# Performance work log

Hardware: AMD Instinct MI355X
Metric: run time of the kernel (lower is better)

The kernel has to match this reference:

```python
import jax, jax.numpy as jnp
import numpy as np

EPS_ATTN = 1e-5   # attention denominator eps (module eps)
EPS_LN = 1e-5     # nn.LayerNorm default eps


def _prime(x, proj):
    # Performer FAVOR+ hyperbolic positive features.
    # x: (B,H,L,dh), proj: (dh,m) -> (B,H,L,2m)
    dn = x.shape[-1] ** -0.25
    xn = dn * x
    d = jnp.einsum('bhld,dm->bhlm', xn, proj)
    diag = 0.5 * jnp.sum(xn * xn, axis=-1, keepdims=True)
    return jnp.concatenate([jnp.exp(d - diag), jnp.exp(-d - diag)], axis=-1)


def setup_inputs() -> dict:
    L, B, H, DH, DM, M = 2048, 4, 8, 64, 512, 256
    key = jax.random.key(0)
    k0, k1, k2 = jax.random.split(key, 3)
    h = jax.random.normal(k0, (L, B, DM), jnp.float32)
    w_qkv = jax.random.normal(k1, (H * 3 * DH, DM), jnp.float32) / np.sqrt(DM)
    w_o = jax.random.normal(k2, (DM, H * DH), jnp.float32) / np.sqrt(H * DH)
    ln_gamma = jnp.ones((DM,), jnp.float32)
    ln_beta = jnp.zeros((DM,), jnp.float32)
    # Gaussian orthogonal random matrix (blockwise QR), rows scaled by sqrt(dh)
    rng = np.random.default_rng(0)
    blocks = []
    for _ in range(M // DH):
        g = rng.standard_normal((DH, DH)).astype(np.float32)
        q, _ = np.linalg.qr(g)
        blocks.append(q.T)
    pm = np.concatenate(blocks, axis=0) * np.sqrt(DH)  # (M, DH)
    proj_matrix = jnp.asarray(pm.T.astype(np.float32))  # (DH, M)
    return {"h": h, "w_qkv": w_qkv, "w_o": w_o,
            "ln_gamma": ln_gamma, "ln_beta": ln_beta,
            "proj_matrix": proj_matrix}


def _forward(h, w_qkv, w_o, ln_gamma, ln_beta, proj_matrix):
    L, B, DM = h.shape
    DH, M = proj_matrix.shape
    H = w_qkv.shape[0] // (3 * DH)
    scale = DH ** -0.5

    qkv = (h @ w_qkv.T).reshape(L, B, H, 3 * DH)
    q, k, v = jnp.split(qkv, 3, axis=-1)
    q = jnp.transpose(q, (1, 2, 0, 3))  # (B,H,L,dh)
    k = jnp.transpose(k, (1, 2, 0, 3))
    v = jnp.transpose(v, (1, 2, 0, 3))

    qp = _prime(q, proj_matrix)  # (B,H,L,2M)
    kp = _prime(k, proj_matrix)
    kp = kp / jnp.sum(kp, axis=-1, keepdims=True)
    qp = qp / jnp.sum(qp, axis=-1, keepdims=True)

    den_acc = jnp.cumsum(kp, axis=2)
    denom = jnp.einsum('bhlm,bhlm->bhl', den_acc, qp)[..., None]  # (B,H,L,1)

    # fast_weight_sum: W_t = W_{t-1} + k_t v_t^T ; out_t = q_t @ W_t
    def step(W, xs):
        qt, kt, vt = xs  # (B,H,2M), (B,H,2M), (B,H,dh)
        W = W + kt[..., :, None] * vt[..., None, :]
        out = jnp.einsum('bhm,bhmd->bhd', qt, W)
        return W, out

    W0 = jnp.zeros((B, H, 2 * M, DH), h.dtype)
    xs = (jnp.transpose(qp, (2, 0, 1, 3)),
          jnp.transpose(kp, (2, 0, 1, 3)),
          jnp.transpose(v, (2, 0, 1, 3)))
    _, out = jax.lax.scan(step, W0, xs)  # (L,B,H,dh)
    out = jnp.transpose(out, (1, 2, 0, 3))  # (B,H,L,dh)

    out = scale * out / (denom + EPS_ATTN)
    out = jnp.transpose(out, (0, 2, 1, 3)).reshape(B, L, H * DH)  # (B,L,H*dh)
    out = jnp.swapaxes(out, 0, 1)  # (L,B,H*dh)

    attn_out = out @ w_o.T
    x = h + attn_out
    mu = jnp.mean(x, axis=-1, keepdims=True)
    var = jnp.mean((x - mu) ** 2, axis=-1, keepdims=True)
    return (x - mu) / jnp.sqrt(var + EPS_LN) * ln_gamma + ln_beta


def reference(h, w_qkv, w_o, ln_gamma, ln_beta, proj_matrix):
    return _forward(h, w_qkv, w_o, ln_gamma, ln_beta, proj_matrix)
```

## Files before the change

### kernel.cpp

```cpp
#include <hip/hip_runtime.h>
#include <hip/hip_fp16.h>
#include <math.h>

#define LSEQ 2048
#define NB 4
#define NH 8
#define DMID 512
#define CHK 128
#define SCALE 0.125f
#define DN 0.35355339059327373f
#define DN2 0.125f
#define EPS_ATTN 1e-5f
#define EPS_LN 1e-5f

typedef _Float16 f16x8 __attribute__((ext_vector_type(8)));
typedef float f32x4 __attribute__((ext_vector_type(4)));

__device__ __forceinline__ void cvt16(const float* __restrict__ p,
                                      _Float16* __restrict__ dst) {
  float4 a = *(const float4*)p, b = *(const float4*)(p + 4);
  float4 c = *(const float4*)(p + 8), d = *(const float4*)(p + 12);
  f16x8 t0 = {(_Float16)a.x, (_Float16)a.y, (_Float16)a.z, (_Float16)a.w,
              (_Float16)b.x, (_Float16)b.y, (_Float16)b.z, (_Float16)b.w};
  f16x8 t1 = {(_Float16)c.x, (_Float16)c.y, (_Float16)c.z, (_Float16)c.w,
              (_Float16)d.x, (_Float16)d.y, (_Float16)d.z, (_Float16)d.w};
  *(f16x8*)dst = t0;
  *(f16x8*)(dst + 8) = t1;
}

__global__ void k_diag(float* out, int n, float val) {
  int i = blockIdx.x * 256 + threadIdx.x;
  if (i < n) out[i] = val;
}

__global__ __launch_bounds__(256) void k_ptr(const float* __restrict__ proj,
                                             __half* __restrict__ projT) {
  int e = blockIdx.x * 256 + threadIdx.x;
  int n = e >> 6, k = e & 63;
  projT[e] = __float2half_rn(proj[k * 256 + n] * DN);
}

__global__ __launch_bounds__(256) void k_qkv(
    const float* __restrict__ A, const float* __restrict__ Wq,
    __half* __restrict__ q, __half* __restrict__ k, __half* __restrict__ v) {
  __shared__ __align__(16) char smem[34816];
  _Float16* Ah = (_Float16*)smem;
  _Float16* Bh = (_Float16*)(smem + 10240);
  _Float16* Oh = (_Float16*)smem;

  const int tid = threadIdx.x;
  const int row0 = blockIdx.x * 128;
  const int col0 = blockIdx.y * 128;
  const int lane = tid & 63, wv = tid >> 6;
  const int ln15 = lane & 15, quad = lane >> 4;
  const int m0 = wv * 32;
  const int srow = tid >> 1, sc = (tid & 1) * 16;

  f32x4 Cacc[2][8];
  const f32x4 z4 = {0.f, 0.f, 0.f, 0.f};
#pragma unroll
  for (int mi = 0; mi < 2; ++mi)
#pragma unroll
    for (int nt = 0; nt < 8; ++nt) Cacc[mi][nt] = z4;

  for (int kt = 0; kt < DMID; kt += 32) {
    cvt16(A + (size_t)(row0 + srow) * DMID + kt + sc, &Ah[srow * 40 + sc]);
    cvt16(Wq + (size_t)(col0 + srow) * DMID + kt + sc, &Bh[srow * 40 + sc]);
    __syncthreads();
    f16x8 a0 = *(const f16x8*)&Ah[(m0 + ln15) * 40 + quad * 8];
    f16x8 a1 = *(const f16x8*)&Ah[(m0 + 16 + ln15) * 40 + quad * 8];
#pragma unroll
    for (int nt = 0; nt < 8; ++nt) {
      f16x8 bf = *(const f16x8*)&Bh[(nt * 16 + ln15) * 40 + quad * 8];
      Cacc[0][nt] = __builtin_amdgcn_mfma_f32_16x16x32_f16(a0, bf, Cacc[0][nt], 0, 0, 0);
      Cacc[1][nt] = __builtin_amdgcn_mfma_f32_16x16x32_f16(a1, bf, Cacc[1][nt], 0, 0, 0);
    }
    __syncthreads();
  }
#pragma unroll
  for (int mi = 0; mi < 2; ++mi)
#pragma unroll
    for (int nt = 0; nt < 8; ++nt)
#pragma unroll
      for (int r = 0; r < 4; ++r)
        Oh[(m0 + mi * 16 + quad * 4 + r) * 136 + nt * 16 + ln15] =
            (_Float16)Cacc[mi][nt][r];
  __syncthreads();
  const int tr = tid >> 4, tc = tid & 15;
  const int col = col0 + tc * 8;
  const int hh = col / 192;
  const int rem = col - hh * 192;
  const int t = rem >> 6;
  const int d0 = rem & 63;
  __half* dstb = (t == 0) ? q : ((t == 1) ? k : v);
#pragma unroll
  for (int i = 0; i < 8; ++i) {
    int lrow = tr * 8 + i;
    int grow = row0 + lrow;
    int l = grow >> 2, bb = grow & 3;
    f16x8 val = *(const f16x8*)&Oh[lrow * 136 + tc * 8];
    *(f16x8*)((_Float16*)dstb + (((size_t)(bb * NH + hh) * LSEQ + l) << 6) + d0) = val;
  }
}

__global__ __launch_bounds__(256) void k_dgemm(
    const __half* __restrict__ qsrc, const __half* __restrict__ ksrc,
    const __half* __restrict__ projT, __half* __restrict__ dqd,
    __half* __restrict__ dkd, float2* __restrict__ nq,
    float2* __restrict__ nk) {
  __shared__ __align__(16) char smem[37888];
  _Float16* Bt = (_Float16*)smem;
  float* g_l  = (float*)(smem + 36864);
  float* ps_l = (float*)(smem + 37376);
  _Float16* Oh = (_Float16*)smem;

  const int tid = threadIdx.x;
  const __half* src = blockIdx.y ? ksrc : qsrc;
  __half* dst = blockIdx.y ? dkd : dqd;
  float2* nrm = blockIdx.y ? nk : nq;
  const size_t r0 = (size_t)blockIdx.x * 128;

  const int lane = tid & 63, wv = tid >> 6;
  const int ln15 = lane & 15, quad = lane >> 4;
  const int m0 = wv * 32;

#pragma unroll
  for (int it = 0; it < 8; ++it) {
    int e = it * 256 + tid;
    int n = e >> 3, seg = e & 7;
    *(f16x8*)&Bt[n * 72 + seg * 8] =
        *(const f16x8*)((const _Float16*)projT + n * 64 + seg * 8);
  }

  f16x8 afrag[2][2];
  float ss[2] = {0.f, 0.f};
#pragma unroll
  for (int mi = 0; mi < 2; ++mi) {
    const _Float16* rp =
        (const _Float16*)src + (r0 + m0 + mi * 16 + ln15) * 64;
#pragma unroll
    for (int ks = 0; ks < 2; ++ks) {
      f16x8 x8 = *(const f16x8*)(rp + ks * 32 + quad * 8);
      afrag[mi][ks] = x8;
#pragma unroll
      for (int j = 0; j < 8; ++j) {
        float xv = (float)x8[j];
        ss[mi] = fmaf(xv, xv, ss[mi]);
      }
    }
    ss[mi] += __shfl_xor(ss[mi], 16);
    ss[mi] += __shfl_xor(ss[mi], 32);
  }
  if (quad == 0) {
    g_l[m0 + ln15] = 0.5f * DN2 * ss[0];
    g_l[m0 + 16 + ln15] = 0.5f * DN2 * ss[1];
  }
  __syncthreads();

  f32x4 Cacc[2][16];
  const f32x4 z4 = {0.f, 0.f, 0.f, 0.f};
#pragma unroll
  for (int mi = 0; mi < 2; ++mi)
#pragma unroll
    for (int nt = 0; nt < 16; ++nt) Cacc[mi][nt] = z4;

#pragma unroll
  for (int ks = 0; ks < 2; ++ks) {
    f16x8 a0 = afrag[0][ks];
    f16x8 a1 = afrag[1][ks];
#pragma unroll
    for (int nt = 0; nt < 16; ++nt) {
      f16x8 bf = *(const f16x8*)&Bt[(nt * 16 + ln15) * 72 + ks * 32 + quad * 8];
      Cacc[0][nt] = __builtin_amdgcn_mfma_f32_16x16x32_f16(a0, bf, Cacc[0][nt], 0, 0, 0);
      Cacc[1][nt] = __builtin_amdgcn_mfma_f32_16x16x32_f16(a1, bf, Cacc[1][nt], 0, 0, 0);
    }
  }

  float gv[2][4], pp[2][4];
#pragma unroll
  for (int mi = 0; mi < 2; ++mi)
#pragma unroll
    for (int r = 0; r < 4; ++r) {
      gv[mi][r] = g_l[m0 + mi * 16 + quad * 4 + r];
      pp[mi][r] = 0.f;
    }
#pragma unroll
  for (int mi = 0; mi < 2; ++mi)
#pragma unroll
    for (int nt = 0; nt < 16; ++nt)
#pragma unroll
      for (int r = 0; r < 4; ++r) {
        float d = Cacc[mi][nt][r];
        pp[mi][r] += __expf(d - gv[mi][r]) + __expf(-d - gv[mi][r]);
      }
#pragma unroll
  for (int mi = 0; mi < 2; ++mi)
#pragma unroll
    for (int r = 0; r < 4; ++r) {
      float p = pp[mi][r];
      p += __shfl_xor(p, 1); p += __shfl_xor(p, 2);
      p += __shfl_xor(p, 4); p += __shfl_xor(p, 8);
      if (ln15 == 0) ps_l[m0 + mi * 16 + quad * 4 + r] = p;
    }

#pragma unroll
  for (int hf = 0; hf < 2; ++hf) {
    __syncthreads();
#pragma unroll
    for (int mi = 0; mi < 2; ++mi)
#pragma unroll
      for (int nt2 = 0; nt2 < 8; ++nt2) {
        int nt = hf * 8 + nt2;
#pragma unroll
        for (int r = 0; r < 4; ++r)
          Oh[(m0 + mi * 16 + quad * 4 + r) * 136 + nt2 * 16 + ln15] =
              (_Float16)Cacc[mi][nt][r];
      }
    __syncthreads();
#pragma unroll
    for (int it = 0; it < 8; ++it) {
      int e = it * 256 + tid;
      int row = e >> 4, seg = e & 15;
      *(f16x8*)((_Float16*)dst + (r0 + row) * 256 + hf * 128 + seg * 8) =
          *(const f16x8*)&Oh[row * 136 + seg * 8];
    }
  }
  if (tid < 128) nrm[r0 + tid] = make_float2(g_l[tid], 1.0f / ps_l[tid]);
}

__global__ __launch_bounds__(256) void k_kv(
    const __half* __restrict__ dk, const float2* __restrict__ nk,
    const __half* __restrict__ v, __half* __restrict__ KV,
    float* __restrict__ Ks) {
  __shared__ __align__(16) char smem[53248];
  _Float16* kpT = (_Float16*)smem;
  _Float16* Vt  = (_Float16*)(smem + 34816);
  float* gk = (float*)(smem + 52224);
  float* ik = (float*)(smem + 52736);
  _Float16* Oh = (_Float16*)smem;

  const int tid = threadIdx.x;
  const int cidx = blockIdx.x;
  const int i0 = blockIdx.y * 128;
  const float fsign = (i0 < 256) ? 1.f : -1.f;
  const int m0col = (i0 < 256) ? i0 : i0 - 256;
  const size_t rowbase = (size_t)cidx * CHK;

  if (tid < 128) {
    float2 n = nk[rowbase + tid];
    gk[tid] = n.x; ik[tid] = n.y;
  }
  __syncthreads();

  {
    const int srow = tid >> 1;
    const int scol = (tid & 1) * 64;
    float g = gk[srow], ivs = ik[srow];
    const _Float16* src =
        (const _Float16*)dk + (rowbase + srow) * 256 + m0col + scol;
#pragma unroll
    for (int it = 0; it < 8; ++it) {
      f16x8 d8 = *(const f16x8*)(src + it * 8);
#pragma unroll
      for (int j = 0; j < 8; ++j)
        kpT[(scol + it * 8 + j) * 136 + srow] =
            (_Float16)(__expf(fsign * (float)d8[j] - g) * ivs);
    }
  }
  {
    int s = tid & 127, dq0 = (tid >> 7) * 32;
    const _Float16* vsrc = (const _Float16*)v + (rowbase + s) * 64 + dq0;
#pragma unroll
    for (int b8 = 0; b8 < 4; ++b8) {
      f16x8 v8 = ((const f16x8*)vsrc)[b8];
#pragma unroll
      for (int j = 0; j < 8; ++j)
        Vt[(dq0 + b8 * 8 + j) * 136 + s] = v8[j];
    }
  }
  __syncthreads();

  const int lane = tid & 63, wv = tid >> 6;
  const int ln15 = lane & 15, quad = lane >> 4;
  const int m0 = wv * 32;

  f32x4 Cacc[2][4], Kacc[2];
  const f32x4 z4 = {0.f, 0.f, 0.f, 0.f};
#pragma unroll
  for (int mi = 0; mi < 2; ++mi) {
#pragma unroll
    for (int nt = 0; nt < 4; ++nt) Cacc[mi][nt] = z4;
    Kacc[mi] = z4;
  }
  f16x8 bone;
#pragma unroll
  for (int j = 0; j < 8; ++j)
    bone[j] = (ln15 == 0) ? (_Float16)1.0f : (_Float16)0.0f;

#pragma unroll
  for (int ks = 0; ks < 4; ++ks) {
    f16x8 a0 = *(const f16x8*)&kpT[(m0 + ln15) * 136 + ks * 32 + quad * 8];
    f16x8 a1 = *(const f16x8*)&kpT[(m0 + 16 + ln15) * 136 + ks * 32 + quad * 8];
#pragma unroll
    for (int nt = 0; nt < 4; ++nt) {
      f16x8 bV = *(const f16x8*)&Vt[(nt * 16 + ln15) * 136 + ks * 32 + quad * 8];
      Cacc[0][nt] = __builtin_amdgcn_mfma_f32_16x16x32_f16(a0, bV, Cacc[0][nt], 0, 0, 0);
      Cacc[1][nt] = __builtin_amdgcn_mfma_f32_16x16x32_f16(a1, bV, Cacc[1][nt], 0, 0, 0);
    }
    Kacc[0] = __builtin_amdgcn_mfma_f32_16x16x32_f16(a0, bone, Kacc[0], 0, 0, 0);
    Kacc[1] = __builtin_amdgcn_mfma_f32_16x16x32_f16(a1, bone, Kacc[1], 0, 0, 0);
  }

  if (ln15 == 0) {
#pragma unroll
    for (int mi = 0; mi < 2; ++mi)
#pragma unroll
      for (int r = 0; r < 4; ++r)
        Ks[(size_t)cidx * 512 + i0 + m0 + mi * 16 + quad * 4 + r] = Kacc[mi][r];
  }
  __syncthreads();
#pragma unroll
  for (int mi = 0; mi < 2; ++mi)
#pragma unroll
    for (int nt = 0; nt < 4; ++nt)
#pragma unroll
      for (int r = 0; r < 4; ++r)
        Oh[(m0 + mi * 16 + quad * 4 + r) * 72 + nt * 16 + ln15] =
            (_Float16)Cacc[mi][nt][r];
  __syncthreads();
#pragma unroll
  for (int it = 0; it < 4; ++it) {
    int e = it * 256 + tid;
    int row = e >> 3, seg = e & 7;
    *(f16x8*)((_Float16*)KV + ((size_t)cidx * 512 + i0 + row) * 64 + seg * 8) =
        *(const f16x8*)&Oh[row * 72 + seg * 8];
  }
}

__global__ __launch_bounds__(256) void k_scan(__half* __restrict__ KV,
                                              float* __restrict__ Ks) {
  const int bh = blockIdx.x;
  const int e0 = blockIdx.y * 4096;
  for (int ee = 0; ee < 16; ++ee) {
    int e = e0 + ee * 256 + threadIdx.x;
    float a = 0.f;
    __half* p = KV + (size_t)bh * 16 * 32768 + e;
#pragma unroll
    for (int c = 0; c < 16; ++c) {
      float vv = __half2float(p[(size_t)c * 32768]);
      p[(size_t)c * 32768] = __float2half_rn(a);
      a += vv;
    }
  }
  if (blockIdx.y == 0) {
    for (int ee = 0; ee < 2; ++ee) {
      int i = ee * 256 + threadIdx.x;
      float a = 0.f;
      float* p = Ks + (size_t)bh * 16 * 512 + i;
#pragma unroll
      for (int c = 0; c < 16; ++c) {
        float vv = p[c * 512];
        p[c * 512] = a;
        a += vv;
      }
    }
  }
}

__global__ __launch_bounds__(256, 2) void k_attn(
    const __half* __restrict__ dq, const __half* __restrict__ dk,
    const float2* __restrict__ nq, const float2* __restrict__ nk,
    const __half* __restrict__ v, const __half* __restrict__ Wpre,
    const float* __restrict__ Kpre, float* __restrict__ outb) {
  __shared__ __align__(16) char smem[55808];
  float* gq_l   = (float*)(smem);
  float* iq_l   = (float*)(smem + 512);
  float* gk_l   = (float*)(smem + 1024);
  float* ik_l   = (float*)(smem + 1536);
  float* den1_l = (float*)(smem + 2048);
  float* den2_l = (float*)(smem + 2560);
  float* invd_l = (float*)(smem + 3072);
  _Float16* qpT = (_Float16*)(smem + 3584);
  _Float16* kpT = (_Float16*)(smem + 13824);
  _Float16* WT  = (_Float16*)(smem + 24064);
  float*    KpT = (float*)(smem + 29184);
  _Float16* S_h = (_Float16*)(smem + 3584);
  _Float16* Vt  = (_Float16*)(smem + 38400);

  const int tid = threadIdx.x;
  const int cidx = blockIdx.x;
  const int cc = cidx & 15, bh = cidx >> 4;
  const size_t rowb = (size_t)cidx * 128;
  const int lane = tid & 63;
  const int wv = tid >> 6;
  const int ln15 = lane & 15;
  const int quad = lane >> 4;
  const int m0 = wv * 32;

  if (tid < 128) {
    float2 n = nq[rowb + tid];
    gq_l[tid] = n.x; iq_l[tid] = n.y;
    float2 n2 = nk[rowb + tid];
    gk_l[tid] = n2.x; ik_l[tid] = n2.y;
  }
  __syncthreads();

  f32x4 Sacc[2][8], Oacc[2][4], Dacc[2];
  const f32x4 z4 = {0.f, 0.f, 0.f, 0.f};
#pragma unroll
  for (int mi = 0; mi < 2; ++mi) {
#pragma unroll
    for (int nt = 0; nt < 8; ++nt) Sacc[mi][nt] = z4;
#pragma unroll
    for (int nt = 0; nt < 4; ++nt) Oacc[mi][nt] = z4;
    Dacc[mi] = z4;
  }

  const int srow = tid >> 1;
  const int sc = (tid & 1) * 16;
  const int wfl = tid >> 3;
  const int wd0 = (tid & 7) * 8;

  for (int kt = 0; kt < 512; kt += 32) {
    const float sgn = (kt < 256) ? 1.f : -1.f;
    const int dc0 = ((kt < 256) ? kt : kt - 256) + sc;
    {
      const _Float16* src = (const _Float16*)dq + (rowb + srow) * 256 + dc0;
      float g = gq_l[srow], iv = iq_l[srow];
      f16x8 d0 = *(const f16x8*)(src);
      f16x8 d1 = *(const f16x8*)(src + 8);
      f16x8 t0, t1;
#pragma unroll
      for (int j = 0; j < 8; ++j) {
        t0[j] = (_Float16)(__expf(sgn * (float)d0[j] - g) * iv);
        t1[j] = (_Float16)(__expf(sgn * (float)d1[j] - g) * iv);
      }
      *(f16x8*)&qpT[srow * 40 + sc] = t0;
      *(f16x8*)&qpT[srow * 40 + sc + 8] = t1;
    }
    {
      const _Float16* src = (const _Float16*)dk + (rowb + srow) * 256 + dc0;
      float g = gk_l[srow], iv = ik_l[srow];
      f16x8 d0 = *(const f16x8*)(src);
      f16x8 d1 = *(const f16x8*)(src + 8);
      f16x8 t0, t1;
#pragma unroll
      for (int j = 0; j < 8; ++j) {
        t0[j] = (_Float16)(__expf(sgn * (float)d0[j] - g) * iv);
        t1[j] = (_Float16)(__expf(sgn * (float)d1[j] - g) * iv);
      }
      *(f16x8*)&kpT[srow * 40 + sc] = t0;
      *(f16x8*)&kpT[srow * 40 + sc + 8] = t1;
    }
    {
      f16x8 wv_ = *(const f16x8*)((const _Float16*)Wpre +
                                  ((size_t)cidx * 512 + kt + wfl) * 64 + wd0);
#pragma unroll
      for (int j = 0; j < 8; ++j) WT[(wd0 + j) * 40 + wfl] = wv_[j];
    }
    if (tid < 32) KpT[tid] = Kpre[(size_t)cidx * 512 + kt + tid];
    __syncthreads();

    f16x8 a0 = *(const f16x8*)&qpT[(m0 + ln15) * 40 + quad * 8];
    f16x8 a1 = *(const f16x8*)&qpT[(m0 + 16 + ln15) * 40 + quad * 8];
#pragma unroll
    for (int nt = 0; nt < 8; ++nt) {
      f16x8 bf = *(const f16x8*)&kpT[(nt * 16 + ln15) * 40 + quad * 8];
      Sacc[0][nt] = __builtin_amdgcn_mfma_f32_16x16x32_f16(a0, bf, Sacc[0][nt], 0, 0, 0);
      Sacc[1][nt] = __builtin_amdgcn_mfma_f32_16x16x32_f16(a1, bf, Sacc[1][nt], 0, 0, 0);
    }
#pragma unroll
    for (int nt = 0; nt < 4; ++nt) {
      f16x8 bw = *(const f16x8*)&WT[(nt * 16 + ln15) * 40 + quad * 8];
      Oacc[0][nt] = __builtin_amdgcn_mfma_f32_16x16x32_f16(a0, bw, Oacc[0][nt], 0, 0, 0);
      Oacc[1][nt] = __builtin_amdgcn_mfma_f32_16x16x32_f16(a1, bw, Oacc[1][nt], 0, 0, 0);
    }
    {
      f16x8 bk;
#pragma unroll
      for (int j = 0; j < 8; ++j)
        bk[j] = (ln15 == 0) ? (_Float16)KpT[quad * 8 + j] : (_Float16)0.f;
      Dacc[0] = __builtin_amdgcn_mfma_f32_16x16x32_f16(a0, bk, Dacc[0], 0, 0, 0);
      Dacc[1] = __builtin_amdgcn_mfma_f32_16x16x32_f16(a1, bk, Dacc[1], 0, 0, 0);
    }
    __syncthreads();
  }

  if (ln15 == 0) {
#pragma unroll
    for (int mi = 0; mi < 2; ++mi)
#pragma unroll
      for (int r = 0; r < 4; ++r)
        den2_l[m0 + mi * 16 + quad * 4 + r] = Dacc[mi][r];
  }
#pragma unroll
  for (int mi = 0; mi < 2; ++mi) {
    float dp[4] = {0.f, 0.f, 0.f, 0.f};
#pragma unroll
    for (int nt = 0; nt < 8; ++nt) {
      int s = nt * 16 + ln15;
#pragma unroll
      for (int r = 0; r < 4; ++r) {
        int tg = m0 + mi * 16 + quad * 4 + r;
        float vsv = (s <= tg) ? Sacc[mi][nt][r] : 0.f;
        dp[r] += vsv;
        S_h[tg * 136 + s] = (_Float16)vsv;
      }
    }
#pragma unroll
    for (int r = 0; r < 4; ++r) {
      float p = dp[r];
      p += __shfl_xor(p, 1); p += __shfl_xor(p, 2);
      p += __shfl_xor(p, 4); p += __shfl_xor(p, 8);
      if (ln15 == 0) den1_l[m0 + mi * 16 + quad * 4 + r] = p;
    }
  }
  __syncthreads();
  if (tid < 128)
    invd_l[tid] = SCALE / (den1_l[tid] + den2_l[tid] + EPS_ATTN);
  {
    int s = tid & 127, d0v = (tid >> 7) * 32;
    const _Float16* vsrc = (const _Float16*)v + (rowb + s) * 64 + d0v;
    f16x8 v0 = ((const f16x8*)vsrc)[0];
    f16x8 v1 = ((const f16x8*)vsrc)[1];
    f16x8 v2 = ((const f16x8*)vsrc)[2];
    f16x8 v3 = ((const f16x8*)vsrc)[3];
#pragma unroll
    for (int j = 0; j < 8; ++j) {
      Vt[(d0v + j) * 136 + s] = v0[j];
      Vt[(d0v + 8 + j) * 136 + s] = v1[j];
      Vt[(d0v + 16 + j) * 136 + s] = v2[j];
      Vt[(d0v + 24 + j) * 136 + s] = v3[j];
    }
  }
  __syncthreads();
#pragma unroll
  for (int ks = 0; ks < 4; ++ks) {
    f16x8 aS0 = *(const f16x8*)&S_h[(m0 + ln15) * 136 + ks * 32 + quad * 8];
    f16x8 aS1 = *(const f16x8*)&S_h[(m0 + 16 + ln15) * 136 + ks * 32 + quad * 8];
#pragma unroll
    for (int nt = 0; nt < 4; ++nt) {
      f16x8 bV = *(const f16x8*)&Vt[(nt * 16 + ln15) * 136 + ks * 32 + quad * 8];
      Oacc[0][nt] = __builtin_amdgcn_mfma_f32_16x16x32_f16(aS0, bV, Oacc[0][nt], 0, 0, 0);
      Oacc[1][nt] = __builtin_amdgcn_mfma_f32_16x16x32_f16(aS1, bV, Oacc[1][nt], 0, 0, 0);
    }
  }
  const int b = bh >> 3, hh = bh & 7;
  float ivv[2][4];
#pragma unroll
  for (int mi = 0; mi < 2; ++mi)
#pragma unroll
    for (int r = 0; r < 4; ++r)
      ivv[mi][r] = invd_l[m0 + mi * 16 + quad * 4 + r];
#pragma unroll
  for (int mi = 0; mi < 2; ++mi)
#pragma unroll
    for (int nt = 0; nt < 4; ++nt) {
      int dcol = nt * 16 + ln15;
#pragma unroll
      for (int r = 0; r < 4; ++r) {
        int t = m0 + mi * 16 + quad * 4 + r;
        int l = cc * 128 + t;
        outb[((size_t)l * 4 + b) * 512 + hh * 64 + dcol] =
            Oacc[mi][nt][r] * ivv[mi][r];
      }
    }
}

__global__ __launch_bounds__(256) void k_oproj(
    const float* __restrict__ A, const float* __restrict__ Wo,
    const float* __restrict__ hres, float* __restrict__ xout) {
  __shared__ __align__(16) char smem[34816];
  _Float16* Ah = (_Float16*)smem;
  _Float16* Bh = (_Float16*)(smem + 10240);
  _Float16* Oh = (_Float16*)smem;

  const int tid = threadIdx.x;
  const int row0 = blockIdx.x * 128;
  const int col0 = blockIdx.y * 128;
  const int lane = tid & 63, wv = tid >> 6;
  const int ln15 = lane & 15, quad = lane >> 4;
  const int m0 = wv * 32;
  const int srow = tid >> 1, sc = (tid & 1) * 16;

  f32x4 Cacc[2][8];
  const f32x4 z4 = {0.f, 0.f, 0.f, 0.f};
#pragma unroll
  for (int mi = 0; mi < 2; ++mi)
#pragma unroll
    for (int nt = 0; nt < 8; ++nt) Cacc[mi][nt] = z4;

  for (int kt = 0; kt < DMID; kt += 32) {
    cvt16(A + (size_t)(row0 + srow) * DMID + kt + sc, &Ah[srow * 40 + sc]);
    cvt16(Wo + (size_t)(col0 + srow) * DMID + kt + sc, &Bh[srow * 40 + sc]);
    __syncthreads();
    f16x8 a0 = *(const f16x8*)&Ah[(m0 + ln15) * 40 + quad * 8];
    f16x8 a1 = *(const f16x8*)&Ah[(m0 + 16 + ln15) * 40 + quad * 8];
#pragma unroll
    for (int nt = 0; nt < 8; ++nt) {
      f16x8 bf = *(const f16x8*)&Bh[(nt * 16 + ln15) * 40 + quad * 8];
      Cacc[0][nt] = __builtin_amdgcn_mfma_f32_16x16x32_f16(a0, bf, Cacc[0][nt], 0, 0, 0);
      Cacc[1][nt] = __builtin_amdgcn_mfma_f32_16x16x32_f16(a1, bf, Cacc[1][nt], 0, 0, 0);
    }
    __syncthreads();
  }
#pragma unroll
  for (int mi = 0; mi < 2; ++mi)
#pragma unroll
    for (int nt = 0; nt < 8; ++nt)
#pragma unroll
      for (int r = 0; r < 4; ++r)
        Oh[(m0 + mi * 16 + quad * 4 + r) * 136 + nt * 16 + ln15] =
            (_Float16)Cacc[mi][nt][r];
  __syncthreads();
  const int tr = tid >> 4, tc = tid & 15;
#pragma unroll
  for (int i = 0; i < 8; ++i) {
    int lrow = tr * 8 + i;
    int grow = row0 + lrow;
    size_t base = (size_t)grow * 512 + col0 + tc * 8;
    f16x8 o = *(const f16x8*)&Oh[lrow * 136 + tc * 8];
    float4 h0 = *(const float4*)(hres + base);
    float4 h1 = *(const float4*)(hres + base + 4);
    *(float4*)(xout + base) =
        make_float4((float)o[0] + h0.x, (float)o[1] + h0.y,
                    (float)o[2] + h0.z, (float)o[3] + h0.w);
    *(float4*)(xout + base + 4) =
        make_float4((float)o[4] + h1.x, (float)o[5] + h1.y,
                    (float)o[6] + h1.z, (float)o[7] + h1.w);
  }
}

__global__ __launch_bounds__(256) void k_ln(float* __restrict__ x,
                                            const float* __restrict__ g,
                                            const float* __restrict__ bta) {
  __shared__ float ws_[4], wq_[4];
  const int row = blockIdx.x;
  const int tid = threadIdx.x;
  float2 vv = *(const float2*)(x + (size_t)row * 512 + tid * 2);
  float s = vv.x + vv.y;
  float sq = vv.x * vv.x + vv.y * vv.y;
#pragma unroll
  for (int off = 1; off < 64; off <<= 1) {
    s += __shfl_xor(s, off, 64);
    sq += __shfl_xor(sq, off, 64);
  }
  if ((tid & 63) == 0) { ws_[tid >> 6] = s; wq_[tid >> 6] = sq; }
  __syncthreads();
  s = ws_[0] + ws_[1] + ws_[2] + ws_[3];
  sq = wq_[0] + wq_[1] + wq_[2] + wq_[3];
  float mu = s * (1.f / 512.f);
  float var = sq * (1.f / 512.f) - mu * mu;
  float rstd = rsqrtf(var + EPS_LN);
  int c = tid * 2;
  float2 o;
  o.x = (vv.x - mu) * rstd * g[c] + bta[c];
  o.y = (vv.y - mu) * rstd * g[c + 1] + bta[c + 1];
  *(float2*)(x + (size_t)row * 512 + c) = o;
}

extern "C" void kernel_launch(void* const* d_in, const int* in_sizes, int n_in,
                              void* d_out, int out_size, void* d_ws,
                              size_t ws_size, hipStream_t stream) {
  const float* h    = (const float*)d_in[0];
  const float* wqkv = (const float*)d_in[1];
  const float* wo   = (const float*)d_in[2];
  const float* g    = (const float*)d_in[3];
  const float* bta  = (const float*)d_in[4];
  const float* proj = (const float*)d_in[5];
  float* out = (float*)d_out;
  char* wsb = (char*)d_ws;

  __half* q   = (__half*)(wsb + 0);
  __half* kb  = (__half*)(wsb + 8388608);
  __half* vb  = (__half*)(wsb + 16777216);
  __half* dq  = (__half*)(wsb + 25165824);
  __half* dk  = (__half*)(wsb + 58720256);
  float2* nq  = (float2*)(wsb + 92274688);
  float2* nk  = (float2*)(wsb + 92798976);
  __half* KV  = (__half*)(wsb + 93323264);
  float*  Ks  = (float*)(wsb + 126877696);
  __half* pT  = (__half*)(wsb + 127926272);
  float* outb = (float*)(wsb + 0);

  if (ws_size < 127959040ull) {
    float val = 1000.0f + (float)(ws_size >> 20);
    k_diag<<<(out_size + 255) / 256, 256, 0, stream>>>(out, out_size, val);
    return;
  }

  k_ptr  <<<dim3(64), 256, 0, stream>>>(proj, pT);
  k_qkv  <<<dim3(64, 12), 256, 0, stream>>>(h, wqkv, q, kb, vb);
  k_dgemm<<<dim3(512, 2), 256, 0, stream>>>(q, kb, pT, dq, dk, nq, nk);
  k_kv   <<<dim3(512, 4), 256, 0, stream>>>(dk, nk, vb, KV, Ks);
  k_scan <<<dim3(32, 8), 256, 0, stream>>>(KV, Ks);
  k_attn <<<dim3(512), 256, 0, stream>>>(dq, dk, nq, nk, vb, KV, Ks, outb);
  k_oproj<<<dim3(64, 4), 256, 0, stream>>>(outb, wo, h, out);
  k_ln   <<<dim3(8192), 256, 0, stream>>>(out, g, bta);
}
```

Baseline: 271.5 us.

## Store V and per-chunk KV state transposed in global memory to skip LDS transposes

The QKV projection now writes V in a transposed (b,h,d,L) layout, and the chunk KV state is stored as (d, m) rows. The kv and attention kernels can then read MFMA B-operands straight from global memory instead of staging and transposing them through shared memory. Shared memory per block shrinks and the launch bounds are raised to 4 blocks per CU for more occupancy. The scan is vectorised to half2. The trade is uncoalesced-ish direct global loads inside MFMA loops in place of LDS reads, and a stray no-op expression was left in the store loop.

```diff
diff --git a/kernel.cpp b/kernel.cpp
--- a/kernel.cpp
+++ b/kernel.cpp
@@ -14,6 +14,7 @@
 #define EPS_LN 1e-5f
 
 typedef _Float16 f16x8 __attribute__((ext_vector_type(8)));
+typedef _Float16 f16x4 __attribute__((ext_vector_type(4)));
 typedef float f32x4 __attribute__((ext_vector_type(4)));
 
 __device__ __forceinline__ void cvt16(const float* __restrict__ p,
@@ -42,7 +43,8 @@
 
 __global__ __launch_bounds__(256) void k_qkv(
     const float* __restrict__ A, const float* __restrict__ Wq,
-    __half* __restrict__ q, __half* __restrict__ k, __half* __restrict__ v) {
+    __half* __restrict__ q, __half* __restrict__ k,
+    __half* __restrict__ VtG) {
   __shared__ __align__(16) char smem[34816];
   _Float16* Ah = (_Float16*)smem;
   _Float16* Bh = (_Float16*)(smem + 10240);
@@ -86,20 +88,48 @@
         Oh[(m0 + mi * 16 + quad * 4 + r) * 136 + nt * 16 + ln15] =
             (_Float16)Cacc[mi][nt][r];
   __syncthreads();
-  const int tr = tid >> 4, tc = tid & 15;
-  const int col = col0 + tc * 8;
-  const int hh = col / 192;
-  const int rem = col - hh * 192;
-  const int t = rem >> 6;
-  const int d0 = rem & 63;
-  __half* dstb = (t == 0) ? q : ((t == 1) ? k : v);
-#pragma unroll
-  for (int i = 0; i < 8; ++i) {
-    int lrow = tr * 8 + i;
-    int grow = row0 + lrow;
-    int l = grow >> 2, bb = grow & 3;
-    f16x8 val = *(const f16x8*)&Oh[lrow * 136 + tc * 8];
-    *(f16x8*)((_Float16*)dstb + (((size_t)(bb * NH + hh) * LSEQ + l) << 6) + d0) = val;
+  {
+    const int tr = tid >> 4, tc = tid & 15;
+    const int col = col0 + tc * 8;
+    const int hh = col / 192;
+    const int rem = col - hh * 192;
+    const int t = rem >> 6;
+    const int d0 = rem & 63;
+    if (t != 2) {
+      __half* dstb = (t == 0) ? q : k;
+#pragma unroll
+      for (int i = 0; i < 8; ++i) {
+        int lrow = tr * 8 + i;
+        int grow = row0 + lrow;
+        int l = grow >> 2, bb = grow & 3;
+        f16x8 val = *(const f16x8*)&Oh[lrow * 136 + tc * 8];
+        *(f16x8*)((_Float16*)k + 0) ;
+        *(f16x8*)((_Float16*)dstb + (((size_t)(bb * NH + hh) * LSEQ + l) << 6) + d0) = val;
+      }
+    }
+  }
+#pragma unroll
+  for (int sg = 0; sg < 2; ++sg) {
+    int cbase = col0 + sg * 64;
+    int hh2 = cbase / 192;
+    int rem2 = cbase - hh2 * 192;
+    if ((rem2 >> 6) != 2) continue;
+    int d = tid >> 2;
+    int b = tid & 3;
+    f16x8 o0, o1, o2, o3;
+#pragma unroll
+    for (int i = 0; i < 8; ++i) {
+      o0[i] = Oh[(4 * (i) + b) * 136 + sg * 64 + d];
+      o1[i] = Oh[(4 * (i + 8) + b) * 136 + sg * 64 + d];
+      o2[i] = Oh[(4 * (i + 16) + b) * 136 + sg * 64 + d];
+      o3[i] = Oh[(4 * (i + 24) + b) * 136 + sg * 64 + d];
+    }
+    size_t base = ((size_t)(b * NH + hh2) * 64 + d) * LSEQ + (row0 >> 2);
+    _Float16* vp = (_Float16*)VtG + base;
+    *(f16x8*)(vp) = o0;
+    *(f16x8*)(vp + 8) = o1;
+    *(f16x8*)(vp + 16) = o2;
+    *(f16x8*)(vp + 24) = o3;
   }
 }
 
@@ -228,16 +258,15 @@
   if (tid < 128) nrm[r0 + tid] = make_float2(g_l[tid], 1.0f / ps_l[tid]);
 }
 
-__global__ __launch_bounds__(256) void k_kv(
+__global__ __launch_bounds__(256, 4) void k_kv(
     const __half* __restrict__ dk, const float2* __restrict__ nk,
-    const __half* __restrict__ v, __half* __restrict__ KV,
+    const __half* __restrict__ VtG, __half* __restrict__ KVt,
     float* __restrict__ Ks) {
-  __shared__ __align__(16) char smem[53248];
+  __shared__ __align__(16) char smem[35840];
   _Float16* kpT = (_Float16*)smem;
-  _Float16* Vt  = (_Float16*)(smem + 34816);
-  float* gk = (float*)(smem + 52224);
-  float* ik = (float*)(smem + 52736);
-  _Float16* Oh = (_Float16*)smem;
+  float* gk = (float*)(smem + 34816);
+  float* ik = (float*)(smem + 35328);
+  _Float16* Oh2 = (_Float16*)smem;
 
   const int tid = threadIdx.x;
   const int cidx = blockIdx.x;
@@ -245,6 +274,7 @@
   const float fsign = (i0 < 256) ? 1.f : -1.f;
   const int m0col = (i0 < 256) ? i0 : i0 - 256;
   const size_t rowbase = (size_t)cidx * CHK;
+  const int bhi = cidx >> 4, cc = cidx & 15;
 
   if (tid < 128) {
     float2 n = nk[rowbase + tid];
@@ -267,17 +297,6 @@
             (_Float16)(__expf(fsign * (float)d8[j] - g) * ivs);
     }
   }
-  {
-    int s = tid & 127, dq0 = (tid >> 7) * 32;
-    const _Float16* vsrc = (const _Float16*)v + (rowbase + s) * 64 + dq0;
-#pragma unroll
-    for (int b8 = 0; b8 < 4; ++b8) {
-      f16x8 v8 = ((const f16x8*)vsrc)[b8];
-#pragma unroll
-      for (int j = 0; j < 8; ++j)
-        Vt[(dq0 + b8 * 8 + j) * 136 + s] = v8[j];
-    }
-  }
   __syncthreads();
 
   const int lane = tid & 63, wv = tid >> 6;
@@ -303,7 +322,9 @@
     f16x8 a1 = *(const f16x8*)&kpT[(m0 + 16 + ln15) * 136 + ks * 32 + quad * 8];
 #pragma unroll
     for (int nt = 0; nt < 4; ++nt) {
-      f16x8 bV = *(const f16x8*)&Vt[(nt * 16 + ln15) * 136 + ks * 32 + quad * 8];
+      f16x8 bV = *(const f16x8*)((const _Float16*)VtG +
+                                 ((size_t)bhi * 64 + nt * 16 + ln15) * LSEQ +
+                                 cc * 128 + ks * 32 + quad * 8);
       Cacc[0][nt] = __builtin_amdgcn_mfma_f32_16x16x32_f16(a0, bV, Cacc[0][nt], 0, 0, 0);
       Cacc[1][nt] = __builtin_amdgcn_mfma_f32_16x16x32_f16(a1, bV, Cacc[1][nt], 0, 0, 0);
     }
@@ -322,34 +343,36 @@
 #pragma unroll
   for (int mi = 0; mi < 2; ++mi)
 #pragma unroll
-    for (int nt = 0; nt < 4; ++nt)
-#pragma unroll
-      for (int r = 0; r < 4; ++r)
-        Oh[(m0 + mi * 16 + quad * 4 + r) * 72 + nt * 16 + ln15] =
-            (_Float16)Cacc[mi][nt][r];
-  __syncthreads();
-#pragma unroll
-  for (int it = 0; it < 4; ++it) {
-    int e = it * 256 + tid;
-    int row = e >> 3, seg = e & 7;
-    *(f16x8*)((_Float16*)KV + ((size_t)cidx * 512 + i0 + row) * 64 + seg * 8) =
-        *(const f16x8*)&Oh[row * 72 + seg * 8];
-  }
-}
-
-__global__ __launch_bounds__(256) void k_scan(__half* __restrict__ KV,
+    for (int nt = 0; nt < 4; ++nt) {
+      f16x4 pack = {(_Float16)Cacc[mi][nt][0], (_Float16)Cacc[mi][nt][1],
+                    (_Float16)Cacc[mi][nt][2], (_Float16)Cacc[mi][nt][3]};
+      *(f16x4*)&Oh2[(nt * 16 + ln15) * 136 + m0 + mi * 16 + quad * 4] = pack;
+    }
+  __syncthreads();
+  {
+    int d = tid >> 2, part = tid & 3;
+    _Float16* dstp =
+        (_Float16*)KVt + (size_t)cidx * 32768 + d * 512 + i0 + part * 32;
+    const _Float16* srcp = &Oh2[d * 136 + part * 32];
+#pragma unroll
+    for (int j = 0; j < 4; ++j)
+      *(f16x8*)(dstp + j * 8) = *(const f16x8*)(srcp + j * 8);
+  }
+}
+
+__global__ __launch_bounds__(256) void k_scan(__half2* __restrict__ KV2,
                                               float* __restrict__ Ks) {
   const int bh = blockIdx.x;
-  const int e0 = blockIdx.y * 4096;
-  for (int ee = 0; ee < 16; ++ee) {
+  const int e0 = blockIdx.y * 2048;
+  for (int ee = 0; ee < 8; ++ee) {
     int e = e0 + ee * 256 + threadIdx.x;
-    float a = 0.f;
-    __half* p = KV + (size_t)bh * 16 * 32768 + e;
+    float ax = 0.f, ay = 0.f;
+    __half2* p = KV2 + (size_t)bh * 16 * 16384 + e;
 #pragma unroll
     for (int c = 0; c < 16; ++c) {
-      float vv = __half2float(p[(size_t)c * 32768]);
-      p[(size_t)c * 32768] = __float2half_rn(a);
-      a += vv;
+      float2 f = __half22float2(p[(size_t)c * 16384]);
+      p[(size_t)c * 16384] = __floats2half2_rn(ax, ay);
+      ax += f.x; ay += f.y;
     }
   }
   if (blockIdx.y == 0) {
@@ -367,25 +390,23 @@
   }
 }
 
-__global__ __launch_bounds__(256, 2) void k_attn(
+__global__ __launch_bounds__(256, 4) void k_attn(
     const __half* __restrict__ dq, const __half* __restrict__ dk,
     const float2* __restrict__ nq, const float2* __restrict__ nk,
-    const __half* __restrict__ v, const __half* __restrict__ Wpre,
+    const __half* __restrict__ VtG, const __half* __restrict__ KVt,
     const float* __restrict__ Kpre, float* __restrict__ outb) {
-  __shared__ __align__(16) char smem[55808];
+  __shared__ __align__(16) char smem[36992];
   float* gq_l   = (float*)(smem);
   float* iq_l   = (float*)(smem + 512);
   float* gk_l   = (float*)(smem + 1024);
   float* ik_l   = (float*)(smem + 1536);
-  float* den1_l = (float*)(smem + 2048);
-  float* den2_l = (float*)(smem + 2560);
-  float* invd_l = (float*)(smem + 3072);
-  _Float16* qpT = (_Float16*)(smem + 3584);
-  _Float16* kpT = (_Float16*)(smem + 13824);
-  _Float16* WT  = (_Float16*)(smem + 24064);
-  float*    KpT = (float*)(smem + 29184);
-  _Float16* S_h = (_Float16*)(smem + 3584);
-  _Float16* Vt  = (_Float16*)(smem + 38400);
+  float* den1_l = (float*)(smem);
+  float* den2_l = (float*)(smem + 512);
+  float* invd_l = (float*)(smem + 1024);
+  float* KpT    = (float*)(smem + 2048);
+  _Float16* qpT = (_Float16*)(smem + 2176);
+  _Float16* kpT = (_Float16*)(smem + 12416);
+  _Float16* S_h = (_Float16*)(smem + 2176);
 
   const int tid = threadIdx.x;
   const int cidx = blockIdx.x;
@@ -418,8 +439,6 @@
 
   const int srow = tid >> 1;
   const int sc = (tid & 1) * 16;
-  const int wfl = tid >> 3;
-  const int wd0 = (tid & 7) * 8;
 
   for (int kt = 0; kt < 512; kt += 32) {
     const float sgn = (kt < 256) ? 1.f : -1.f;
@@ -452,12 +471,6 @@
       *(f16x8*)&kpT[srow * 40 + sc] = t0;
       *(f16x8*)&kpT[srow * 40 + sc + 8] = t1;
     }
-    {
-      f16x8 wv_ = *(const f16x8*)((const _Float16*)Wpre +
-                                  ((size_t)cidx * 512 + kt + wfl) * 64 + wd0);
-#pragma unroll
-      for (int j = 0; j < 8; ++j) WT[(wd0 + j) * 40 + wfl] = wv_[j];
-    }
     if (tid < 32) KpT[tid] = Kpre[(size_t)cidx * 512 + kt + tid];
     __syncthreads();
 
@@ -471,7 +484,9 @@
     }
 #pragma unroll
     for (int nt = 0; nt < 4; ++nt) {
-      f16x8 bw = *(const f16x8*)&WT[(nt * 16 + ln15) * 40 + quad * 8];
+      f16x8 bw = *(const f16x8*)((const _Float16*)KVt +
+                                 (size_t)cidx * 32768 +
+                                 (nt * 16 + ln15) * 512 + kt + quad * 8);
       Oacc[0][nt] = __builtin_amdgcn_mfma_f32_16x16x32_f16(a0, bw, Oacc[0][nt], 0, 0, 0);
       Oacc[1][nt] = __builtin_amdgcn_mfma_f32_16x16x32_f16(a1, bw, Oacc[1][nt], 0, 0, 0);
     }
@@ -518,21 +533,6 @@
   __syncthreads();
   if (tid < 128)
     invd_l[tid] = SCALE / (den1_l[tid] + den2_l[tid] + EPS_ATTN);
-  {
-    int s = tid & 127, d0v = (tid >> 7) * 32;
-    const _Float16* vsrc = (const _Float16*)v + (rowb + s) * 64 + d0v;
-    f16x8 v0 = ((const f16x8*)vsrc)[0];
-    f16x8 v1 = ((const f16x8*)vsrc)[1];
-    f16x8 v2 = ((const f16x8*)vsrc)[2];
-    f16x8 v3 = ((const f16x8*)vsrc)[3];
-#pragma unroll
-    for (int j = 0; j < 8; ++j) {
-      Vt[(d0v + j) * 136 + s] = v0[j];
-      Vt[(d0v + 8 + j) * 136 + s] = v1[j];
-      Vt[(d0v + 16 + j) * 136 + s] = v2[j];
-      Vt[(d0v + 24 + j) * 136 + s] = v3[j];
-    }
-  }
   __syncthreads();
 #pragma unroll
   for (int ks = 0; ks < 4; ++ks) {
@@ -540,7 +540,9 @@
     f16x8 aS1 = *(const f16x8*)&S_h[(m0 + 16 + ln15) * 136 + ks * 32 + quad * 8];
 #pragma unroll
     for (int nt = 0; nt < 4; ++nt) {
-      f16x8 bV = *(const f16x8*)&Vt[(nt * 16 + ln15) * 136 + ks * 32 + quad * 8];
+      f16x8 bV = *(const f16x8*)((const _Float16*)VtG +
+                                 ((size_t)bh * 64 + nt * 16 + ln15) * LSEQ +
+                                 cc * 128 + ks * 32 + quad * 8);
       Oacc[0][nt] = __builtin_amdgcn_mfma_f32_16x16x32_f16(aS0, bV, Oacc[0][nt], 0, 0, 0);
       Oacc[1][nt] = __builtin_amdgcn_mfma_f32_16x16x32_f16(aS1, bV, Oacc[1][nt], 0, 0, 0);
     }
@@ -673,12 +675,12 @@
 
   __half* q   = (__half*)(wsb + 0);
   __half* kb  = (__half*)(wsb + 8388608);
-  __half* vb  = (__half*)(wsb + 16777216);
+  __half* VtG = (__half*)(wsb + 16777216);
   __half* dq  = (__half*)(wsb + 25165824);
   __half* dk  = (__half*)(wsb + 58720256);
   float2* nq  = (float2*)(wsb + 92274688);
   float2* nk  = (float2*)(wsb + 92798976);
-  __half* KV  = (__half*)(wsb + 93323264);
+  __half* KVt = (__half*)(wsb + 93323264);
   float*  Ks  = (float*)(wsb + 126877696);
   __half* pT  = (__half*)(wsb + 127926272);
   float* outb = (float*)(wsb + 0);
@@ -690,11 +692,11 @@
   }
 
   k_ptr  <<<dim3(64), 256, 0, stream>>>(proj, pT);
-  k_qkv  <<<dim3(64, 12), 256, 0, stream>>>(h, wqkv, q, kb, vb);
+  k_qkv  <<<dim3(64, 12), 256, 0, stream>>>(h, wqkv, q, kb, VtG);
   k_dgemm<<<dim3(512, 2), 256, 0, stream>>>(q, kb, pT, dq, dk, nq, nk);
-  k_kv   <<<dim3(512, 4), 256, 0, stream>>>(dk, nk, vb, KV, Ks);
-  k_scan <<<dim3(32, 8), 256, 0, stream>>>(KV, Ks);
-  k_attn <<<dim3(512), 256, 0, stream>>>(dq, dk, nq, nk, vb, KV, Ks, outb);
+  k_kv   <<<dim3(512, 4), 256, 0, stream>>>(dk, nk, VtG, KVt, Ks);
+  k_scan <<<dim3(32, 8), 256, 0, stream>>>((__half2*)KVt, Ks);
+  k_attn <<<dim3(512), 256, 0, stream>>>(dq, dk, nq, nk, VtG, KVt, Ks, outb);
   k_oproj<<<dim3(64, 4), 256, 0, stream>>>(outb, wo, h, out);
   k_ln   <<<dim3(8192), 256, 0, stream>>>(out, g, bta);
 }
```

After: 327.0 us. 1.2x slower.
